# Kernel tuning notes

Measured on AMD Instinct MI355X. Metric: run time of the kernel, lower is better.

Reference implementation:

```python
import jax, jax.numpy as jnp
import numpy as np

QUERY_DIM = 512
HEADS = 8
DIM_HEAD = 64
INNER = HEADS * DIM_HEAD  # 512


def setup_inputs() -> dict:
    key = jax.random.key(0)
    ks = jax.random.split(key, 7)
    B, N, M = 4, 2048, 2048
    s = 0.02
    return {
        "x": jax.random.normal(ks[0], (B, N, QUERY_DIM), dtype=jnp.float32),
        "context": jax.random.normal(ks[1], (B, M, QUERY_DIM), dtype=jnp.float32),
        "Wq": jax.random.normal(ks[2], (QUERY_DIM, INNER), dtype=jnp.float32) * s,
        "Wk": jax.random.normal(ks[3], (QUERY_DIM, INNER), dtype=jnp.float32) * s,
        "Wv": jax.random.normal(ks[4], (QUERY_DIM, INNER), dtype=jnp.float32) * s,
        "Wo": jax.random.normal(ks[5], (INNER, QUERY_DIM), dtype=jnp.float32) * s,
        "bo": jnp.zeros((QUERY_DIM,), dtype=jnp.float32),
    }


def reference(x, context, Wq, Wk, Wv, Wo, bo):
    B, N, _ = x.shape
    M = context.shape[1]
    # projections, split heads: [B, H, N, D]
    q = (x @ Wq).reshape(B, N, HEADS, DIM_HEAD).transpose(0, 2, 1, 3)
    k = (context @ Wk).reshape(B, M, HEADS, DIM_HEAD).transpose(0, 2, 1, 3)
    v = (context @ Wv).reshape(B, M, HEADS, DIM_HEAD).transpose(0, 2, 1, 3)
    scale = 1.0 / jnp.sqrt(jnp.float32(DIM_HEAD))
    attn = jnp.einsum('bhid,bhjd->bhij', q, k) * scale  # [B,H,N,M]
    attn = jax.nn.softmax(attn, axis=-1)
    out = jnp.einsum('bhij,bhjd->bhid', attn, v)  # [B,H,N,D]
    out = out.transpose(0, 2, 1, 3).reshape(B, N, INNER)
    return out @ Wo + bo
```

## Files before the change

kernel.cpp:

```cpp
#include <hip/hip_runtime.h>


typedef short bf16x8 __attribute__((ext_vector_type(8)));
typedef float f32x4 __attribute__((ext_vector_type(4)));
typedef float f32x16 __attribute__((ext_vector_type(16)));
typedef unsigned int u32x4 __attribute__((ext_vector_type(4)));

#define NB 4
#define NN 2048
#define QD 512
#define DH 64
#define QSCALE 0.18033688011112042f

__device__ __forceinline__ unsigned short f2bf(float f) {
  unsigned u = __float_as_uint(f);
  unsigned r = (u + 0x7fffu + ((u >> 16) & 1u)) >> 16;
  return (unsigned short)r;
}

__device__ __forceinline__ unsigned cvtpk(float a, float b) {
  unsigned r;
  asm("v_cvt_pk_bf16_f32 %0, %1, %2" : "=v"(r) : "v"(a), "v"(b));
  return r;
}

__device__ __forceinline__ void pl32swap(unsigned& a, unsigned& b) {
  asm("v_permlane32_swap_b32 %0, %1" : "+v"(a), "+v"(b));
}

__device__ __forceinline__ void gload16(const void* g, void* l) {
  __builtin_amdgcn_global_load_lds((const __attribute__((address_space(1))) unsigned int*)g,
                                   (__attribute__((address_space(3))) unsigned int*)l, 16, 0, 0);
}

__global__ __launch_bounds__(256) void cvt_weights(const float* __restrict__ Wq, const float* __restrict__ Wk,
                                                   const float* __restrict__ Wv, const float* __restrict__ Wo,
                                                   unsigned short* __restrict__ wqt, unsigned short* __restrict__ wkt,
                                                   unsigned short* __restrict__ wvt, unsigned short* __restrict__ wot) {
  __shared__ float t[32][33];
  const float* W = blockIdx.z == 0 ? Wq : blockIdx.z == 1 ? Wk : blockIdx.z == 2 ? Wv : Wo;
  unsigned short* O = blockIdx.z == 0 ? wqt : blockIdx.z == 1 ? wkt : blockIdx.z == 2 ? wvt : wot;
  int c0 = blockIdx.x * 32, k0 = blockIdx.y * 32;
  int tx = threadIdx.x, ty = threadIdx.y;
#pragma unroll
  for (int j = 0; j < 4; j++) t[ty + 8 * j][tx] = W[(k0 + ty + 8 * j) * QD + c0 + tx];
  __syncthreads();
#pragma unroll
  for (int j = 0; j < 4; j++) O[(c0 + ty + 8 * j) * QD + k0 + tx] = f2bf(t[tx][ty + 8 * j]);
}

__global__ __launch_bounds__(256, 2) void qkv_gemm(const float* __restrict__ x, const float* __restrict__ ctx,
                                                   const unsigned short* __restrict__ wqt,
                                                   const unsigned short* __restrict__ wkt,
                                                   const unsigned short* __restrict__ wvt,
                                                   unsigned short* __restrict__ q_ws,
                                                   unsigned short* __restrict__ k_ws,
                                                   unsigned short* __restrict__ v_ws) {
  __shared__ __align__(16) unsigned short sA[128 * 64];
  __shared__ __align__(16) unsigned short sB[128 * 64];
  const int z = blockIdx.z;
  const float* A = (z == 0) ? x : ctx;
  const unsigned short* Bt = (z == 0) ? wqt : (z == 1) ? wkt : wvt;
  const int lane = threadIdx.x & 63, wid = threadIdx.x >> 6;
  const int lo = lane & 15, hi = lane >> 4;
  const int wm = wid >> 1, wn = wid & 1;
  const int r0 = blockIdx.x * 128, c0 = blockIdx.y * 128;
  const int r8 = lane >> 3, c8l = lane & 7;
  f32x4 acc[4][4] = {};
  for (int k0 = 0; k0 < QD; k0 += 64) {
    __syncthreads();
#pragma unroll
    for (int i = 0; i < 4; i++) {
      int id = i * 256 + threadIdx.x;
      int row = id >> 3, ks = id & 7;
      const float* ap = &A[(r0 + row) * QD + k0 + ks * 8];
      float4 a = *(const float4*)ap;
      float4 b = *(const float4*)(ap + 4);
      u32x4 w = {cvtpk(a.x, a.y), cvtpk(a.z, a.w), cvtpk(b.x, b.y), cvtpk(b.z, b.w)};
      *(u32x4*)((char*)sA + id * 16) = w;
      int chunk = wid * 4 + i;
      int brow = chunk * 8 + r8;
      gload16(&Bt[(c0 + brow) * QD + k0 + c8l * 8], (char*)sB + chunk * 1024);
    }
    __syncthreads();
#pragma unroll
    for (int kk = 0; kk < 2; kk++) {
      bf16x8 af[4], bfr[4];
#pragma unroll
      for (int t = 0; t < 4; t++) af[t] = *(const bf16x8*)&sA[(wm * 64 + t * 16 + lo) * 64 + (kk * 4 + hi) * 8];
#pragma unroll
      for (int u = 0; u < 4; u++) bfr[u] = *(const bf16x8*)&sB[(wn * 64 + u * 16 + lo) * 64 + (kk * 4 + hi) * 8];
#pragma unroll
      for (int t = 0; t < 4; t++)
#pragma unroll
        for (int u = 0; u < 4; u++)
          acc[t][u] = __builtin_amdgcn_mfma_f32_16x16x32_bf16(af[t], bfr[u], acc[t][u], 0, 0, 0);
    }
  }
  const float outscale = (z == 0) ? QSCALE : 1.0f;
  unsigned short* Cq = (z == 0) ? q_ws : k_ws;
#pragma unroll
  for (int t = 0; t < 4; t++)
#pragma unroll
    for (int u = 0; u < 4; u++)
#pragma unroll
      for (int ri = 0; ri < 4; ri++) {
        int r = r0 + wm * 64 + t * 16 + hi * 4 + ri;
        int c = c0 + wn * 64 + u * 16 + lo;
        float v = acc[t][u][ri] * outscale;
        int b = r >> 11, n = r & 2047, h = c >> 6, d = c & 63;
        if (z == 2)
          v_ws[(((b << 3) | h) * DH + d) * NN + n] = f2bf(v);
        else
          Cq[(((b << 3) | h) * NN + n) * DH + d] = f2bf(v);
      }
}

__global__ __launch_bounds__(512, 4) void flash_attn(const unsigned short* __restrict__ Q,
                                                     const unsigned short* __restrict__ K,
                                                     const unsigned short* __restrict__ Vt,
                                                     unsigned short* __restrict__ po,
                                                     float* __restrict__ pml) {
  __shared__ __align__(16) char sKV[2][16384];
  const int tid = threadIdx.x;
  const int lane = tid & 63, wid = tid >> 6;
  const int l31 = lane & 31, hi = lane >> 5;
  const int bh = blockIdx.x, half = blockIdx.z;
  const int bhK = bh * NN, bhV = bh * DH;
  const int kv0 = half * (NN / 2);
  const int qrow = blockIdx.y * 256 + wid * 32 + l31;
  po += half * (32 * 2048 * 64);
  pml += half * (32 * 2048);

  bf16x8 qf[4];
#pragma unroll
  for (int ks = 0; ks < 4; ks++)
    qf[ks] = *(const bf16x8*)&Q[(bhK + qrow) * DH + ks * 16 + hi * 8];

  const int row_s = tid >> 3, slot_s = tid & 7;
  const int swz = (slot_s ^ (row_s & 7)) * 8;

#define STAGE(J0, BUF)                                                     \
  do {                                                                     \
    char* b_ = (char*)sKV[BUF];                                            \
    gload16(&K[(bhK + (J0) + row_s) * DH + swz], b_ + wid * 1024);         \
    gload16(&Vt[(bhV + row_s) * NN + (J0) + swz], b_ + 8192 + wid * 1024); \
  } while (0)

  float l = 0.f;
  f32x16 o[2] = {};

  STAGE(kv0, 0);

  for (int it = 0; it < 16; ++it) {
    asm volatile("s_waitcnt vmcnt(0)" ::: "memory");
    __builtin_amdgcn_s_barrier();
    __builtin_amdgcn_sched_barrier(0);
    if (it + 1 < 16) STAGE(kv0 + (it + 1) * 64, (it + 1) & 1);
    const char* buf = (const char*)sKV[it & 1];

    f32x16 st[2] = {};
    __builtin_amdgcn_s_setprio(1);
#pragma unroll
    for (int g = 0; g < 2; g++)
#pragma unroll
      for (int ks = 0; ks < 4; ks++) {
        bf16x8 kf = *(const bf16x8*)(buf + (g * 32 + l31) * 128 + (((ks * 2 + hi) ^ (l31 & 7)) << 4));
        st[g] = __builtin_amdgcn_mfma_f32_32x32x16_bf16(kf, qf[ks], st[g], 0, 0, 0);
      }
    __builtin_amdgcn_s_setprio(0);

#pragma unroll
    for (int g = 0; g < 2; g++)
#pragma unroll
      for (int c = 0; c < 16; c++) st[g][c] = __builtin_amdgcn_exp2f(st[g][c]);
    float s8[8];
#pragma unroll
    for (int c = 0; c < 8; c++) s8[c] = (st[0][c] + st[0][c + 8]) + (st[1][c] + st[1][c + 8]);
#pragma unroll
    for (int w = 4; w >= 1; w >>= 1)
#pragma unroll
      for (int c = 0; c < 4; c++)
        if (c < w) s8[c] += s8[c + w];
    l += s8[0] + __shfl_xor(s8[0], 32);

    bf16x8 pf[2][2];
#pragma unroll
    for (int g = 0; g < 2; g++)
#pragma unroll
      for (int s = 0; s < 2; s++) {
        const int cb = s * 8;
        unsigned a0 = cvtpk(st[g][cb + 0], st[g][cb + 1]);
        unsigned a1 = cvtpk(st[g][cb + 2], st[g][cb + 3]);
        unsigned b0 = cvtpk(st[g][cb + 4], st[g][cb + 5]);
        unsigned b1 = cvtpk(st[g][cb + 6], st[g][cb + 7]);
        pl32swap(a0, b0);
        pl32swap(a1, b1);
        union { unsigned u[4]; bf16x8 v; } pu;
        pu.u[0] = a0; pu.u[1] = a1; pu.u[2] = b0; pu.u[3] = b1;
        pf[g][s] = pu.v;
      }

    __builtin_amdgcn_s_setprio(1);
#pragma unroll
    for (int dt = 0; dt < 2; dt++)
#pragma unroll
      for (int g = 0; g < 2; g++)
#pragma unroll
        for (int s = 0; s < 2; s++) {
          int row = dt * 32 + l31;
          bf16x8 vf = *(const bf16x8*)(buf + 8192 + row * 128 + (((g * 4 + s * 2 + hi) ^ (row & 7)) << 4));
          o[dt] = __builtin_amdgcn_mfma_f32_32x32x16_bf16(vf, pf[g][s], o[dt], 0, 0, 0);
        }
    __builtin_amdgcn_s_setprio(0);
  }
#undef STAGE

  float inv = 1.f / l;
  const int rbase = (bh * 2048 + qrow) * 64;
#pragma unroll
  for (int dt = 0; dt < 2; dt++)
#pragma unroll
    for (int cg = 0; cg < 4; cg++) {
      ushort4 w;
      w.x = f2bf(o[dt][cg * 4 + 0] * inv);
      w.y = f2bf(o[dt][cg * 4 + 1] * inv);
      w.z = f2bf(o[dt][cg * 4 + 2] * inv);
      w.w = f2bf(o[dt][cg * 4 + 3] * inv);
      int d0 = dt * 32 + cg * 8 + hi * 4;
      *(ushort4*)&po[rbase + d0] = w;
    }
  if (hi == 0) pml[bh * 2048 + qrow] = l;
}

__global__ __launch_bounds__(256, 2) void out_gemm(const unsigned short* __restrict__ po,
                                                   const float* __restrict__ pml,
                                                   const unsigned short* __restrict__ Bt,
                                                   float* __restrict__ out,
                                                   const float* __restrict__ bias) {
  __shared__ __align__(16) unsigned short sA[128 * 64];
  __shared__ __align__(16) unsigned short sB[64 * 64];
  const unsigned short* po1 = po + 32 * 2048 * 64;
  const float* pml1 = pml + 32 * 2048;
  const int lane = threadIdx.x & 63, wid = threadIdx.x >> 6;
  const int lo = lane & 15, hi = lane >> 4;
  const int wm = wid >> 1, wn = wid & 1;
  const int r0 = blockIdx.x * 128, c0 = blockIdx.y * 64;
  const int r8 = lane >> 3, c8l = lane & 7;
  f32x4 acc[4][2] = {};
  for (int k0 = 0; k0 < QD; k0 += 64) {
    __syncthreads();
    const int h = k0 >> 6;
#pragma unroll
    for (int i = 0; i < 4; i++) {
      int id = i * 256 + threadIdx.x;
      int row = id >> 3, slot = id & 7;
      int r = r0 + row, b = r >> 11, n = r & 2047;
      int pr = ((b << 3) | h) * NN + n;
      float la = pml[pr], lb = pml1[pr];
      float s = __builtin_amdgcn_rcpf(la + lb);
      float wa = la * s, wb = lb * s;
      u32x4 A0 = *(const u32x4*)&po[pr * 64 + slot * 8];
      u32x4 A1 = *(const u32x4*)&po1[pr * 64 + slot * 8];
      u32x4 res;
#pragma unroll
      for (int j = 0; j < 4; j++) {
        float a_lo = __uint_as_float(A0[j] << 16), a_hi = __uint_as_float(A0[j] & 0xffff0000u);
        float b_lo = __uint_as_float(A1[j] << 16), b_hi = __uint_as_float(A1[j] & 0xffff0000u);
        res[j] = cvtpk(a_lo * wa + b_lo * wb, a_hi * wa + b_hi * wb);
      }
      *(u32x4*)((char*)sA + id * 16) = res;
    }
#pragma unroll
    for (int i = 0; i < 2; i++) {
      int chunk = wid * 2 + i;
      int row = chunk * 8 + r8;
      gload16(&Bt[(c0 + row) * QD + k0 + c8l * 8], (char*)sB + chunk * 1024);
    }
    __syncthreads();
#pragma unroll
    for (int kk = 0; kk < 2; kk++) {
      bf16x8 af[4], bfr[2];
#pragma unroll
      for (int t = 0; t < 4; t++) af[t] = *(const bf16x8*)&sA[(wm * 64 + t * 16 + lo) * 64 + (kk * 4 + hi) * 8];
#pragma unroll
      for (int u = 0; u < 2; u++) bfr[u] = *(const bf16x8*)&sB[(wn * 32 + u * 16 + lo) * 64 + (kk * 4 + hi) * 8];
#pragma unroll
      for (int t = 0; t < 4; t++)
#pragma unroll
        for (int u = 0; u < 2; u++)
          acc[t][u] = __builtin_amdgcn_mfma_f32_16x16x32_bf16(af[t], bfr[u], acc[t][u], 0, 0, 0);
    }
  }
#pragma unroll
  for (int t = 0; t < 4; t++)
#pragma unroll
    for (int u = 0; u < 2; u++)
#pragma unroll
      for (int ri = 0; ri < 4; ri++) {
        int r = r0 + wm * 64 + t * 16 + hi * 4 + ri;
        int c = c0 + wn * 32 + u * 16 + lo;
        out[r * QD + c] = acc[t][u][ri] + bias[c];
      }
}

extern "C" void kernel_launch(void* const* d_in, const int* in_sizes, int n_in,
                              void* d_out, int out_size, void* d_ws, size_t ws_size,
                              hipStream_t stream) {
  const float* x   = (const float*)d_in[0];
  const float* ctx = (const float*)d_in[1];
  const float* Wq  = (const float*)d_in[2];
  const float* Wk  = (const float*)d_in[3];
  const float* Wv  = (const float*)d_in[4];
  const float* Wo  = (const float*)d_in[5];
  const float* bo  = (const float*)d_in[6];
  char* ws = (char*)d_ws;

  unsigned short* wqt  = (unsigned short*)(ws);
  unsigned short* wkt  = (unsigned short*)(ws + 524288);
  unsigned short* wvt  = (unsigned short*)(ws + 1048576);
  unsigned short* wot  = (unsigned short*)(ws + 1572864);
  unsigned short* q_ws = (unsigned short*)(ws + 2097152);
  unsigned short* k_ws = (unsigned short*)(ws + 10485760);
  unsigned short* v_ws = (unsigned short*)(ws + 18874368);
  unsigned short* po   = (unsigned short*)(ws + 27262976);
  float*          pml  = (float*)(ws + 44040192);
  float* out = (float*)d_out;

  cvt_weights<<<dim3(16, 16, 4), dim3(32, 8), 0, stream>>>(Wq, Wk, Wv, Wo, wqt, wkt, wvt, wot);

  qkv_gemm<<<dim3(64, 4, 3), 256, 0, stream>>>(x, ctx, wqt, wkt, wvt, q_ws, k_ws, v_ws);

  flash_attn<<<dim3(32, 8, 2), 512, 0, stream>>>(q_ws, k_ws, v_ws, po, pml);

  out_gemm<<<dim3(64, 8), 256, 0, stream>>>(po, pml, wot, out, bo);
}
```

Measured before the change: 105.6 us.

## Pre-convert activations to bf16 and double-buffer QKV GEMM with async LDS loads

```diff
diff --git a/kernel.cpp b/kernel.cpp
--- a/kernel.cpp
+++ b/kernel.cpp
@@ -31,6 +31,24 @@
 __device__ __forceinline__ void gload16(const void* g, void* l) {
   __builtin_amdgcn_global_load_lds((const __attribute__((address_space(1))) unsigned int*)g,
                                    (__attribute__((address_space(3))) unsigned int*)l, 16, 0, 0);
+}
+
+__global__ __launch_bounds__(256) void cvt_inputs(const float* __restrict__ x,
+                                                  const float* __restrict__ ctx,
+                                                  unsigned short* __restrict__ xb,
+                                                  unsigned short* __restrict__ cb) {
+  int i = blockIdx.x * 256 + threadIdx.x;
+  const int total = (NB * NN * QD) / 4;
+  if (i < total) {
+    float4 v = ((const float4*)x)[i];
+    ushort4 o;
+    o.x = f2bf(v.x); o.y = f2bf(v.y); o.z = f2bf(v.z); o.w = f2bf(v.w);
+    ((ushort4*)xb)[i] = o;
+    float4 w = ((const float4*)ctx)[i];
+    ushort4 p;
+    p.x = f2bf(w.x); p.y = f2bf(w.y); p.z = f2bf(w.z); p.w = f2bf(w.w);
+    ((ushort4*)cb)[i] = p;
+  }
 }
 
 __global__ __launch_bounds__(256) void cvt_weights(const float* __restrict__ Wq, const float* __restrict__ Wk,
@@ -49,40 +67,45 @@
   for (int j = 0; j < 4; j++) O[(c0 + ty + 8 * j) * QD + k0 + tx] = f2bf(t[tx][ty + 8 * j]);
 }
 
-__global__ __launch_bounds__(256, 2) void qkv_gemm(const float* __restrict__ x, const float* __restrict__ ctx,
+__global__ __launch_bounds__(256, 2) void qkv_gemm(const unsigned short* __restrict__ xb,
+                                                   const unsigned short* __restrict__ cb,
                                                    const unsigned short* __restrict__ wqt,
                                                    const unsigned short* __restrict__ wkt,
                                                    const unsigned short* __restrict__ wvt,
                                                    unsigned short* __restrict__ q_ws,
                                                    unsigned short* __restrict__ k_ws,
                                                    unsigned short* __restrict__ v_ws) {
-  __shared__ __align__(16) unsigned short sA[128 * 64];
-  __shared__ __align__(16) unsigned short sB[128 * 64];
+  __shared__ __align__(16) char sAB[2][32768];
   const int z = blockIdx.z;
-  const float* A = (z == 0) ? x : ctx;
+  const unsigned short* A = (z == 0) ? xb : cb;
   const unsigned short* Bt = (z == 0) ? wqt : (z == 1) ? wkt : wvt;
   const int lane = threadIdx.x & 63, wid = threadIdx.x >> 6;
   const int lo = lane & 15, hi = lane >> 4;
   const int wm = wid >> 1, wn = wid & 1;
-  const int r0 = blockIdx.x * 128, c0 = blockIdx.y * 128;
+  const int c0 = blockIdx.x * 128, r0 = blockIdx.y * 128;
   const int r8 = lane >> 3, c8l = lane & 7;
+
+#define STAGEQ(K0, BUF)                                                      \
+  do {                                                                       \
+    char* b_ = sAB[BUF];                                                     \
+    _Pragma("unroll") for (int i_ = 0; i_ < 4; ++i_) {                       \
+      int chunk_ = wid * 4 + i_;                                             \
+      int row_ = chunk_ * 8 + r8;                                            \
+      gload16(&A[(r0 + row_) * QD + (K0) + c8l * 8], b_ + chunk_ * 1024);    \
+      gload16(&Bt[(c0 + row_) * QD + (K0) + c8l * 8],                        \
+              b_ + 16384 + chunk_ * 1024);                                   \
+    }                                                                        \
+  } while (0)
+
   f32x4 acc[4][4] = {};
-  for (int k0 = 0; k0 < QD; k0 += 64) {
-    __syncthreads();
-#pragma unroll
-    for (int i = 0; i < 4; i++) {
-      int id = i * 256 + threadIdx.x;
-      int row = id >> 3, ks = id & 7;
-      const float* ap = &A[(r0 + row) * QD + k0 + ks * 8];
-      float4 a = *(const float4*)ap;
-      float4 b = *(const float4*)(ap + 4);
-      u32x4 w = {cvtpk(a.x, a.y), cvtpk(a.z, a.w), cvtpk(b.x, b.y), cvtpk(b.z, b.w)};
-      *(u32x4*)((char*)sA + id * 16) = w;
-      int chunk = wid * 4 + i;
-      int brow = chunk * 8 + r8;
-      gload16(&Bt[(c0 + brow) * QD + k0 + c8l * 8], (char*)sB + chunk * 1024);
-    }
-    __syncthreads();
+  STAGEQ(0, 0);
+  for (int ks = 0; ks < 8; ++ks) {
+    asm volatile("s_waitcnt vmcnt(0)" ::: "memory");
+    __builtin_amdgcn_s_barrier();
+    __builtin_amdgcn_sched_barrier(0);
+    if (ks + 1 < 8) STAGEQ((ks + 1) * 64, (ks + 1) & 1);
+    const unsigned short* sA = (const unsigned short*)sAB[ks & 1];
+    const unsigned short* sB = sA + 8192;
 #pragma unroll
     for (int kk = 0; kk < 2; kk++) {
       bf16x8 af[4], bfr[4];
@@ -97,6 +120,7 @@
           acc[t][u] = __builtin_amdgcn_mfma_f32_16x16x32_bf16(af[t], bfr[u], acc[t][u], 0, 0, 0);
     }
   }
+#undef STAGEQ
   const float outscale = (z == 0) ? QSCALE : 1.0f;
   unsigned short* Cq = (z == 0) ? q_ws : k_ws;
 #pragma unroll
@@ -316,20 +340,23 @@
   const float* bo  = (const float*)d_in[6];
   char* ws = (char*)d_ws;
 
-  unsigned short* wqt  = (unsigned short*)(ws);
-  unsigned short* wkt  = (unsigned short*)(ws + 524288);
-  unsigned short* wvt  = (unsigned short*)(ws + 1048576);
-  unsigned short* wot  = (unsigned short*)(ws + 1572864);
-  unsigned short* q_ws = (unsigned short*)(ws + 2097152);
-  unsigned short* k_ws = (unsigned short*)(ws + 10485760);
-  unsigned short* v_ws = (unsigned short*)(ws + 18874368);
-  unsigned short* po   = (unsigned short*)(ws + 27262976);
+  unsigned short* xb   = (unsigned short*)(ws);
+  unsigned short* cb   = (unsigned short*)(ws + 8388608);
+  unsigned short* po   = (unsigned short*)(ws);
+  unsigned short* wqt  = (unsigned short*)(ws + 16777216);
+  unsigned short* wkt  = (unsigned short*)(ws + 17301504);
+  unsigned short* wvt  = (unsigned short*)(ws + 17825792);
+  unsigned short* wot  = (unsigned short*)(ws + 18350080);
+  unsigned short* q_ws = (unsigned short*)(ws + 18874368);
+  unsigned short* k_ws = (unsigned short*)(ws + 27262976);
+  unsigned short* v_ws = (unsigned short*)(ws + 35651584);
   float*          pml  = (float*)(ws + 44040192);
   float* out = (float*)d_out;
 
+  cvt_inputs<<<4096, 256, 0, stream>>>(x, ctx, xb, cb);
   cvt_weights<<<dim3(16, 16, 4), dim3(32, 8), 0, stream>>>(Wq, Wk, Wv, Wo, wqt, wkt, wvt, wot);
 
-  qkv_gemm<<<dim3(64, 4, 3), 256, 0, stream>>>(x, ctx, wqt, wkt, wvt, q_ws, k_ws, v_ws);
+  qkv_gemm<<<dim3(4, 64, 3), 256, 0, stream>>>(xb, cb, wqt, wkt, wvt, q_ws, k_ws, v_ws);
 
   flash_attn<<<dim3(32, 8, 2), 512, 0, stream>>>(q_ws, k_ws, v_ws, po, pml);
 
```

Result: slower. 112.2 us (+6.2%).
